# Kernel tuning notes

Measured on AMD Instinct MI355X. Metric: run time of the kernel, lower is better.

The kernel has to match this reference:

```python
import jax, jax.numpy as jnp
import numpy as np

KSIZE = 5
DILATION = 1
DYN = 32  # dynamic (value) channels


def setup_inputs() -> dict:
    key = jax.random.key(0)
    k1, k2 = jax.random.split(key)
    x = jax.random.normal(k1, (4, 64, 256, 256), dtype=jnp.float32)
    kernel = jax.random.normal(k2, (KSIZE * KSIZE, 1), dtype=jnp.float32)
    return {"input": x, "kernel": kernel}


def _neighborhoods(x):
    """Gather KxK dilated neighborhoods with zero padding.
    x: [B, C, H, W] -> [B, C, K^2, H, W], taps in row-major (i, j) order
    matching nn.Unfold."""
    B, C, H, W = x.shape
    pad = DILATION * (KSIZE // 2)
    xp = jnp.pad(x, ((0, 0), (0, 0), (pad, pad), (pad, pad)))
    taps = [xp[:, :, i * DILATION:i * DILATION + H, j * DILATION:j * DILATION + W]
            for i in range(KSIZE) for j in range(KSIZE)]
    return jnp.stack(taps, axis=2)


def reference(input, kernel):
    x = input
    nbrs = _neighborhoods(x)                      # [B, C, K2, H, W]
    # scores over static channels (c >= DYN) against center pixel, scaled by
    # learned per-tap kernel weight / kernel_size
    scores = jnp.einsum('bckhw,bchw->bkhw', nbrs[:, DYN:], x[:, DYN:])
    scores = scores * (kernel[:, 0][None, :, None, None] / KSIZE)
    smax = jax.nn.softmax(scores, axis=1)          # softmax over K^2 taps
    # weighted sum of dynamic channels
    out = jnp.einsum('bkhw,bckhw->bchw', smax, nbrs[:, :DYN])
    return out
```

## Files before the change

kernel.cpp:

```cpp
#include <hip/hip_runtime.h>
#include <math.h>

#define KS    5
#define K2    25
#define DYN   32
#define BB    4
#define HH    256
#define WW    256
#define PLANE (HH * WW)
#define LROW  264
#define TROWS 6
#define NCH   4
#define CHBLK (TROWS * LROW + 8)
#define NTHR  256

typedef const __attribute__((address_space(1))) void* gas_t;
typedef __attribute__((address_space(3))) void*       las_t;

__global__ __launch_bounds__(NTHR, 2)
void local_attn_kernel(const float* __restrict__ x,
                       const float* __restrict__ kern,
                       float* __restrict__ out)
{
    __shared__ __align__(16) float lds[2][NCH][CHBLK];
    __shared__ float kw[K2];

    const int tid = threadIdx.x;
    for (int i = tid; i < 2 * NCH * CHBLK; i += NTHR) ((float*)lds)[i] = 0.0f;
    if (tid < K2) kw[tid] = kern[tid] * (1.0f / KS);

    const int lane = tid & 63;
    const int wv   = tid >> 6;
    const int ty   = wv >> 1;
    const int cg   = lane >> 5;
    const int tx   = ((wv & 1) << 5) | (lane & 31);
    const int w0   = tx << 2;

    const int bx     = blockIdx.x;
    const int hgroup = ((bx & 7) << 4) | (bx >> 3);
    const int h0     = hgroup * 2;
    const int b      = blockIdx.y;
    const int h      = h0 + ty;

    const float* xb = x + (size_t)b * 64 * PLANE;

    bool rok[TROWS]; int roff[TROWS];
#pragma unroll
    for (int j = 0; j < TROWS; ++j) {
        const int r = h0 - 2 + j;
        rok[j]  = (unsigned)r < (unsigned)HH;
        roff[j] = r * WW;
    }

    auto stagein = [&](int bufi, int chbase) {
        const float* cp = xb + (size_t)(chbase + wv) * PLANE;
#pragma unroll
        for (int j = 0; j < TROWS; ++j) {
            if (rok[j]) {
                __builtin_amdgcn_global_load_lds(
                    (gas_t)(const void*)(cp + roff[j] + 4 * lane),
                    (las_t)(void*)(&lds[bufi][wv][j * LROW + 4]),
                    16, 0, 0);
            }
        }
    };

    float s[4][K2];
#pragma unroll
    for (int p = 0; p < 4; ++p)
#pragma unroll
        for (int k = 0; k < K2; ++k) s[p][k] = 0.0f;

    auto compute_score = [&](int bufi) {
#pragma unroll
        for (int dch = 0; dch < 2; ++dch) {
            const int cl = cg * 2 + dch;
            const float* cb = &lds[bufi][cl][0];
            float ctr[4];
            {
                const float* rp = cb + (ty + 2) * LROW + w0;
                float4 a = *(const float4*)(rp);
                float4 m = *(const float4*)(rp + 4);
                float4 c = *(const float4*)(rp + 8);
                float f[12] = {a.x,a.y,a.z,a.w, m.x,m.y,m.z,m.w, c.x,c.y,c.z,c.w};
                ctr[0]=f[4]; ctr[1]=f[5]; ctr[2]=f[6]; ctr[3]=f[7];
#pragma unroll
                for (int j = 0; j < KS; ++j)
#pragma unroll
                    for (int p = 0; p < 4; ++p)
                        s[p][2*KS+j] = fmaf(f[p+j+2], ctr[p], s[p][2*KS+j]);
            }
#pragma unroll
            for (int i = 0; i < KS; ++i) {
                if (i == 2) continue;
                const float* rp = cb + (ty + i) * LROW + w0;
                float4 a = *(const float4*)(rp);
                float4 m = *(const float4*)(rp + 4);
                float4 c = *(const float4*)(rp + 8);
                float f[12] = {a.x,a.y,a.z,a.w, m.x,m.y,m.z,m.w, c.x,c.y,c.z,c.w};
#pragma unroll
                for (int j = 0; j < KS; ++j)
#pragma unroll
                    for (int p = 0; p < 4; ++p)
                        s[p][i*KS+j] = fmaf(f[p+j+2], ctr[p], s[p][i*KS+j]);
            }
        }
    };

    auto compute_out = [&](int bufi, int chbase) {
#pragma unroll
        for (int dch = 0; dch < 2; ++dch) {
            const int cl = cg * 2 + dch;
            const float* cb = &lds[bufi][cl][0];
            float acc[4] = {0.f, 0.f, 0.f, 0.f};
#pragma unroll
            for (int i = 0; i < KS; ++i) {
                const float* rp = cb + (ty + i) * LROW + w0;
                float4 a = *(const float4*)(rp);
                float4 m = *(const float4*)(rp + 4);
                float4 c = *(const float4*)(rp + 8);
                float f[12] = {a.x,a.y,a.z,a.w, m.x,m.y,m.z,m.w, c.x,c.y,c.z,c.w};
#pragma unroll
                for (int j = 0; j < KS; ++j)
#pragma unroll
                    for (int p = 0; p < 4; ++p)
                        acc[p] = fmaf(f[p+j+2], s[p][i*KS+j], acc[p]);
            }
            *(float4*)(out + ((size_t)b * DYN + chbase + cl) * PLANE + h * WW + w0)
                = make_float4(acc[0], acc[1], acc[2], acc[3]);
        }
    };

    __syncthreads();
    stagein(0, 32);
    __syncthreads();

#pragma unroll 1
    for (int t = 0; t < 16; ++t) {
        if (t + 1 < 16)
            stagein((t + 1) & 1, (t + 1 < 8) ? 32 + 4 * (t + 1) : 4 * (t + 1 - 8));
        if (t < 8) {
            compute_score(t & 1);
            if (t == 7) {
#pragma unroll
                for (int p = 0; p < 4; ++p)
#pragma unroll
                    for (int k = 0; k < K2; ++k)
                        s[p][k] += __shfl_xor(s[p][k], 32, 64);
#pragma unroll
                for (int p = 0; p < 4; ++p) {
                    float mx = -INFINITY;
#pragma unroll
                    for (int k = 0; k < K2; ++k) {
                        float v = s[p][k] * kw[k];
                        s[p][k] = v;
                        mx = fmaxf(mx, v);
                    }
                    float sum = 0.0f;
#pragma unroll
                    for (int k = 0; k < K2; ++k) {
                        float e = __expf(s[p][k] - mx);
                        s[p][k] = e;
                        sum += e;
                    }
                    const float inv = 1.0f / sum;
#pragma unroll
                    for (int k = 0; k < K2; ++k) s[p][k] *= inv;
                }
            }
        } else {
            compute_out(t & 1, 4 * (t - 8));
        }
        __syncthreads();
    }
}

extern "C" void kernel_launch(void* const* d_in, const int* in_sizes, int n_in,
                              void* d_out, int out_size, void* d_ws, size_t ws_size,
                              hipStream_t stream) {
    const float* x    = (const float*)d_in[0];
    const float* kern = (const float*)d_in[1];
    float*       out  = (float*)d_out;

    dim3 grid(HH / 2, BB, 1);
    dim3 block(NTHR, 1, 1);
    hipLaunchKernelGGL(local_attn_kernel, grid, block, 0, stream, x, kern, out);
}
```

Measured before the change: 126.1 us.

## Stage channel pairs as packed fp16 in LDS and use dot2 for scores

```diff
diff --git a/kernel.cpp b/kernel.cpp
--- a/kernel.cpp
+++ b/kernel.cpp
@@ -3,30 +3,41 @@
 
 #define KS    5
 #define K2    25
-#define DYN   32
 #define BB    4
 #define HH    256
 #define WW    256
 #define PLANE (HH * WW)
-#define LROW  264
-#define TROWS 6
-#define NCH   4
-#define CHBLK (TROWS * LROW + 8)
+#define LROWD 264
+#define PTILE 1864
 #define NTHR  256
 
-typedef const __attribute__((address_space(1))) void* gas_t;
-typedef __attribute__((address_space(3))) void*       las_t;
+typedef __attribute__((ext_vector_type(2))) _Float16 half2_t;
+
+static __device__ __forceinline__ half2_t u2h(unsigned u) { return __builtin_bit_cast(half2_t, u); }
+
+static __device__ __forceinline__ unsigned pkrtz(float a, float b) {
+    auto h = __builtin_amdgcn_cvt_pkrtz(a, b);
+    return __builtin_bit_cast(unsigned, h);
+}
+
+static __device__ __forceinline__ float dot2(half2_t a, half2_t b, float c) {
+#if __has_builtin(__builtin_amdgcn_fdot2)
+    return __builtin_amdgcn_fdot2(a, b, c, false);
+#else
+    return (float)a.x * (float)b.x + ((float)a.y * (float)b.y + c);
+#endif
+}
 
 __global__ __launch_bounds__(NTHR, 2)
 void local_attn_kernel(const float* __restrict__ x,
                        const float* __restrict__ kern,
                        float* __restrict__ out)
 {
-    __shared__ __align__(16) float lds[2][NCH][CHBLK];
+    __shared__ unsigned ldsu[2 * 4 * PTILE];
     __shared__ float kw[K2];
 
     const int tid = threadIdx.x;
-    for (int i = tid; i < 2 * NCH * CHBLK; i += NTHR) ((float*)lds)[i] = 0.0f;
+    for (int i = tid; i < 2 * 4 * PTILE; i += NTHR) ldsu[i] = 0u;
     if (tid < K2) kw[tid] = kern[tid] * (1.0f / KS);
 
     const int lane = tid & 63;
@@ -39,109 +50,97 @@
     const int bx     = blockIdx.x;
     const int hgroup = ((bx & 7) << 4) | (bx >> 3);
     const int h0     = hgroup * 2;
+    const int h      = h0 + ty;
     const int b      = blockIdx.y;
-    const int h      = h0 + ty;
 
     const float* xb = x + (size_t)b * 64 * PLANE;
 
-    bool rok[TROWS]; int roff[TROWS];
-#pragma unroll
-    for (int j = 0; j < TROWS; ++j) {
-        const int r = h0 - 2 + j;
-        rok[j]  = (unsigned)r < (unsigned)HH;
-        roff[j] = r * WW;
+    int gofs[6], lofs[6], pofs[6];
+#pragma unroll
+    for (int i = 0; i < 6; ++i) {
+        const int rp   = (tid >> 6) + 4 * i;
+        const int row  = rp % 6;
+        const int pair = rp / 6;
+        const int r    = h0 - 2 + row;
+        const bool v   = (unsigned)r < (unsigned)HH;
+        gofs[i] = min(max(r, 0), HH - 1) * WW + (tid & 63) * 4;
+        pofs[i] = pair * 2 * PLANE;
+        lofs[i] = pair * PTILE + (v ? row : 6) * LROWD + 2 + (tid & 63) * 4;
     }
 
-    auto stagein = [&](int bufi, int chbase) {
-        const float* cp = xb + (size_t)(chbase + wv) * PLANE;
-#pragma unroll
-        for (int j = 0; j < TROWS; ++j) {
-            if (rok[j]) {
-                __builtin_amdgcn_global_load_lds(
-                    (gas_t)(const void*)(cp + roff[j] + 4 * lane),
-                    (las_t)(void*)(&lds[bufi][wv][j * LROW + 4]),
-                    16, 0, 0);
+    float4 pa[6], pb[6];
+    auto prefetch = [&](int st) {
+        const float* xc = xb + (size_t)((st < 4) ? 32 + st * 8 : (st - 4) * 8) * PLANE;
+#pragma unroll
+        for (int i = 0; i < 6; ++i) {
+            pa[i] = *(const float4*)(xc + pofs[i] + gofs[i]);
+            pb[i] = *(const float4*)(xc + pofs[i] + PLANE + gofs[i]);
+        }
+    };
+    auto cvtwrite = [&](int bufi) {
+        unsigned* lb = ldsu + bufi * 4 * PTILE;
+#pragma unroll
+        for (int i = 0; i < 6; ++i) {
+            const unsigned d0 = pkrtz(pa[i].x, pb[i].x);
+            const unsigned d1 = pkrtz(pa[i].y, pb[i].y);
+            const unsigned d2 = pkrtz(pa[i].z, pb[i].z);
+            const unsigned d3 = pkrtz(pa[i].w, pb[i].w);
+            *(uint2*)(lb + lofs[i])     = make_uint2(d0, d1);
+            *(uint2*)(lb + lofs[i] + 2) = make_uint2(d2, d3);
+        }
+    };
+
+    float s[4][K2];
+#pragma unroll
+    for (int p = 0; p < 4; ++p)
+#pragma unroll
+        for (int k = 0; k < K2; ++k) s[p][k] = 0.0f;
+
+    __syncthreads();
+    prefetch(0);
+    cvtwrite(0);
+    __syncthreads();
+
+#pragma unroll 1
+    for (int t = 0; t < 8; ++t) {
+        if (t + 1 < 8) prefetch(t + 1);
+        const unsigned* buf = ldsu + (t & 1) * 4 * PTILE;
+
+        if (t < 4) {
+#pragma unroll
+            for (int dp = 0; dp < 2; ++dp) {
+                const unsigned* tb = buf + (cg * 2 + dp) * PTILE;
+                half2_t ctr[4];
+                {
+                    const unsigned* rp = tb + (ty + 2) * LROWD + w0;
+                    const uint4 r0 = *(const uint4*)(rp);
+                    const uint4 r1 = *(const uint4*)(rp + 4);
+                    half2_t f[8] = {u2h(r0.x), u2h(r0.y), u2h(r0.z), u2h(r0.w),
+                                    u2h(r1.x), u2h(r1.y), u2h(r1.z), u2h(r1.w)};
+#pragma unroll
+                    for (int p = 0; p < 4; ++p) ctr[p] = f[p + 2];
+#pragma unroll
+                    for (int j = 0; j < KS; ++j)
+#pragma unroll
+                        for (int p = 0; p < 4; ++p)
+                            s[p][2 * KS + j] = dot2(f[p + j], ctr[p], s[p][2 * KS + j]);
+                }
+#pragma unroll
+                for (int i = 0; i < KS; ++i) {
+                    if (i == 2) continue;
+                    const unsigned* rp = tb + (ty + i) * LROWD + w0;
+                    const uint4 r0 = *(const uint4*)(rp);
+                    const uint4 r1 = *(const uint4*)(rp + 4);
+                    half2_t f[8] = {u2h(r0.x), u2h(r0.y), u2h(r0.z), u2h(r0.w),
+                                    u2h(r1.x), u2h(r1.y), u2h(r1.z), u2h(r1.w)};
+#pragma unroll
+                    for (int j = 0; j < KS; ++j)
+#pragma unroll
+                        for (int p = 0; p < 4; ++p)
+                            s[p][i * KS + j] = dot2(f[p + j], ctr[p], s[p][i * KS + j]);
+                }
             }
-        }
-    };
-
-    float s[4][K2];
-#pragma unroll
-    for (int p = 0; p < 4; ++p)
-#pragma unroll
-        for (int k = 0; k < K2; ++k) s[p][k] = 0.0f;
-
-    auto compute_score = [&](int bufi) {
-#pragma unroll
-        for (int dch = 0; dch < 2; ++dch) {
-            const int cl = cg * 2 + dch;
-            const float* cb = &lds[bufi][cl][0];
-            float ctr[4];
-            {
-                const float* rp = cb + (ty + 2) * LROW + w0;
-                float4 a = *(const float4*)(rp);
-                float4 m = *(const float4*)(rp + 4);
-                float4 c = *(const float4*)(rp + 8);
-                float f[12] = {a.x,a.y,a.z,a.w, m.x,m.y,m.z,m.w, c.x,c.y,c.z,c.w};
-                ctr[0]=f[4]; ctr[1]=f[5]; ctr[2]=f[6]; ctr[3]=f[7];
-#pragma unroll
-                for (int j = 0; j < KS; ++j)
-#pragma unroll
-                    for (int p = 0; p < 4; ++p)
-                        s[p][2*KS+j] = fmaf(f[p+j+2], ctr[p], s[p][2*KS+j]);
-            }
-#pragma unroll
-            for (int i = 0; i < KS; ++i) {
-                if (i == 2) continue;
-                const float* rp = cb + (ty + i) * LROW + w0;
-                float4 a = *(const float4*)(rp);
-                float4 m = *(const float4*)(rp + 4);
-                float4 c = *(const float4*)(rp + 8);
-                float f[12] = {a.x,a.y,a.z,a.w, m.x,m.y,m.z,m.w, c.x,c.y,c.z,c.w};
-#pragma unroll
-                for (int j = 0; j < KS; ++j)
-#pragma unroll
-                    for (int p = 0; p < 4; ++p)
-                        s[p][i*KS+j] = fmaf(f[p+j+2], ctr[p], s[p][i*KS+j]);
-            }
-        }
-    };
-
-    auto compute_out = [&](int bufi, int chbase) {
-#pragma unroll
-        for (int dch = 0; dch < 2; ++dch) {
-            const int cl = cg * 2 + dch;
-            const float* cb = &lds[bufi][cl][0];
-            float acc[4] = {0.f, 0.f, 0.f, 0.f};
-#pragma unroll
-            for (int i = 0; i < KS; ++i) {
-                const float* rp = cb + (ty + i) * LROW + w0;
-                float4 a = *(const float4*)(rp);
-                float4 m = *(const float4*)(rp + 4);
-                float4 c = *(const float4*)(rp + 8);
-                float f[12] = {a.x,a.y,a.z,a.w, m.x,m.y,m.z,m.w, c.x,c.y,c.z,c.w};
-#pragma unroll
-                for (int j = 0; j < KS; ++j)
-#pragma unroll
-                    for (int p = 0; p < 4; ++p)
-                        acc[p] = fmaf(f[p+j+2], s[p][i*KS+j], acc[p]);
-            }
-            *(float4*)(out + ((size_t)b * DYN + chbase + cl) * PLANE + h * WW + w0)
-                = make_float4(acc[0], acc[1], acc[2], acc[3]);
-        }
-    };
-
-    __syncthreads();
-    stagein(0, 32);
-    __syncthreads();
-
-#pragma unroll 1
-    for (int t = 0; t < 16; ++t) {
-        if (t + 1 < 16)
-            stagein((t + 1) & 1, (t + 1 < 8) ? 32 + 4 * (t + 1) : 4 * (t + 1 - 8));
-        if (t < 8) {
-            compute_score(t & 1);
-            if (t == 7) {
+            if (t == 3) {
 #pragma unroll
                 for (int p = 0; p < 4; ++p)
 #pragma unroll
@@ -169,9 +168,40 @@
                 }
             }
         } else {
-            compute_out(t & 1, 4 * (t - 8));
-        }
-        __syncthreads();
+            const int chb = (t - 4) * 8;
+#pragma unroll
+            for (int dp = 0; dp < 2; ++dp) {
+                const unsigned* tb = buf + (cg * 2 + dp) * PTILE;
+                float alo[4] = {0.f, 0.f, 0.f, 0.f};
+                float ahi[4] = {0.f, 0.f, 0.f, 0.f};
+#pragma unroll
+                for (int i = 0; i < KS; ++i) {
+                    const unsigned* rp = tb + (ty + i) * LROWD + w0;
+                    const uint4 r0 = *(const uint4*)(rp);
+                    const uint4 r1 = *(const uint4*)(rp + 4);
+                    half2_t f[8] = {u2h(r0.x), u2h(r0.y), u2h(r0.z), u2h(r0.w),
+                                    u2h(r1.x), u2h(r1.y), u2h(r1.z), u2h(r1.w)};
+#pragma unroll
+                    for (int j = 0; j < KS; ++j)
+#pragma unroll
+                        for (int p = 0; p < 4; ++p) {
+                            const half2_t v = f[p + j];
+                            const float  wgt = s[p][i * KS + j];
+                            alo[p] = fmaf((float)v.x, wgt, alo[p]);
+                            ahi[p] = fmaf((float)v.y, wgt, ahi[p]);
+                        }
+                }
+                const int c0 = chb + (cg * 2 + dp) * 2;
+                float* op = out + ((size_t)b * 32 + c0) * PLANE + h * WW + w0;
+                *(float4*)op           = make_float4(alo[0], alo[1], alo[2], alo[3]);
+                *(float4*)(op + PLANE) = make_float4(ahi[0], ahi[1], ahi[2], ahi[3]);
+            }
+        }
+
+        if (t + 1 < 8) {
+            cvtwrite((t + 1) & 1);
+            __syncthreads();
+        }
     }
 }
 
```

Measured after the change: 113.7 us. 9.9% less time.
